# Kernel tuning notes

Hardware: AMD Instinct MI355X
Metric: run time of the kernel (lower is better)

## Reference

```python
import jax, jax.numpy as jnp
import numpy as np

B = 4096   # batch (samples)
V = 64     # num_vars
H = 512    # hidden_dim


def setup_inputs() -> dict:
    key = jax.random.key(0)
    k0, k1, k2, k3 = jax.random.split(key, 4)
    x = jax.random.normal(k0, (B, V), dtype=jnp.float32)
    # learned params: adjacency logits + stacked per-variable 2-layer MLPs
    adj_weights = jax.random.normal(k1, (V, V), dtype=jnp.float32) * 0.1
    W1 = jax.random.normal(k2, (V, V - 1, H), dtype=jnp.float32) * (1.0 / np.sqrt(V - 1))
    b1 = jnp.zeros((V, H), dtype=jnp.float32)
    W2 = jax.random.normal(k3, (V, H), dtype=jnp.float32) * (1.0 / np.sqrt(H))
    b2 = jnp.zeros((V,), dtype=jnp.float32)
    return {"x": x, "adj_weights": adj_weights, "W1": W1, "b1": b1, "W2": W2, "b2": b2}


def reference(x, adj_weights, W1, b1, W2, b2):
    Vn = adj_weights.shape[0]
    # sigmoid adjacency with zeroed diagonal
    adj = jax.nn.sigmoid(adj_weights) * (1.0 - jnp.eye(Vn, dtype=adj_weights.dtype))
    # idx[i, j] = j if j < i else j + 1  -> columns of x excluding variable i
    j = jnp.arange(Vn - 1)
    idx = j[None, :] + (j[None, :] >= jnp.arange(Vn)[:, None])  # [V, V-1] int
    gathered = x[:, idx]                                  # [B, V, V-1]
    w = jnp.take_along_axis(adj, idx, axis=1)             # [V, V-1] (row i, cols != i)
    weighted = gathered * w[None, :, :]                   # [B, V, V-1]
    # batched small MLP per variable
    h = jax.nn.relu(jnp.einsum('bvk,vkh->bvh', weighted, W1) + b1[None])  # [B, V, H]
    out = jnp.einsum('bvh,vh->bv', h, W2) + b2[None]                      # [B, V]
    return out
```

## Files before the change

### kernel.cpp

```cpp
#include <hip/hip_runtime.h>
#include <hip/hip_bf16.h>

constexpr int Bn = 4096;
constexpr int Vn = 64;
constexpr int Hn = 512;

typedef __attribute__((ext_vector_type(8))) short bf16x8;
typedef __attribute__((ext_vector_type(4))) float f32x4;
typedef __attribute__((ext_vector_type(8))) unsigned short u16x8;

union bfcast { u16x8 u; bf16x8 b; };

__device__ __forceinline__ unsigned short f2bf(float f) {
    union { float f; unsigned int u; } x; x.f = f;
    unsigned int u = x.u;
    u += 0x7fffu + ((u >> 16) & 1u);
    return (unsigned short)(u >> 16);
}

__global__ void prep_w1(const float* __restrict__ adjw,
                        const float* __restrict__ W1,
                        unsigned short* __restrict__ bfrag) {
    int nb   = (blockIdx.x & 7) * 128 + (blockIdx.x >> 3);
    int tid  = nb * 256 + threadIdx.x;
    int lane = tid & 63;
    int ks   = (tid >> 6) & 1;
    int nt   = (tid >> 7) & 31;
    int v    = tid >> 12;

    int n     = nt * 16 + (lane & 15);
    int kbase = ks * 32 + ((lane >> 4) << 3);

    u16x8 o;
#pragma unroll
    for (int e = 0; e < 8; ++e) {
        int k = kbase + e;
        float val = 0.f;
        if (k != v) {
            float aw = adjw[v * Vn + k];
            float s  = 1.f / (1.f + __expf(-aw));
            int  j   = k - (k > v);
            val = s * W1[((size_t)(v * (Vn - 1) + j)) * Hn + n];
        }
        o[e] = f2bf(val);
    }
    *reinterpret_cast<u16x8*>(bfrag + (size_t)tid * 8) = o;
}

__global__ __launch_bounds__(256, 4)
void main_k(const float* __restrict__ x,
            const unsigned short* __restrict__ bfrag,
            const float* __restrict__ b1, const float* __restrict__ W2,
            const float* __restrict__ b2, float* __restrict__ out) {
    int wid  = threadIdx.x >> 6;
    int lane = threadIdx.x & 63;
    int nb   = (blockIdx.x & 7) * 128 + (blockIdx.x >> 3);
    int job  = nb * 4 + wid;
    int v    = job >> 6;
    int rg   = job & 63;

    const unsigned short* bpan = bfrag + (size_t)v * 32 * 2 * 512;
    const float* w2row = W2 + v * Hn;
    const float* b1row = b1 + v * Hn;
    int ncol = lane & 15;

    bf16x8 pb0[3], pb1[3];
    float  pw2[3], pbv[3];
#pragma unroll
    for (int p = 0; p < 3; ++p) {
        pb0[p] = *reinterpret_cast<const bf16x8*>(bpan + (size_t)p * 1024 + 0 + lane * 8);
        pb1[p] = *reinterpret_cast<const bf16x8*>(bpan + (size_t)p * 1024 + 512 + lane * 8);
        pw2[p] = w2row[p * 16 + ncol];
        pbv[p] = b1row[p * 16 + ncol];
    }

    bf16x8 a[4][2];
#pragma unroll
    for (int m = 0; m < 4; ++m)
#pragma unroll
        for (int ks = 0; ks < 2; ++ks) {
            int brow  = rg * 64 + m * 16 + (lane & 15);
            int kbase = ks * 32 + ((lane >> 4) << 3);
            const float* xp = x + (size_t)brow * Vn + kbase;
            f32x4 lo = *reinterpret_cast<const f32x4*>(xp);
            f32x4 hi = *reinterpret_cast<const f32x4*>(xp + 4);
            bfcast t;
#pragma unroll
            for (int e = 0; e < 4; ++e) {
                t.u[e]     = f2bf(lo[e]);
                t.u[e + 4] = f2bf(hi[e]);
            }
            a[m][ks] = t.b;
        }

    float partial[4][4] = {};

#pragma unroll
    for (int j = 0; j < 32; ++j) {
        const int cur = j % 3;
        if (j < 29) {
            const int nxt = j % 3;
        }
#pragma unroll
        for (int m = 0; m < 4; ++m) {
            f32x4 c = {pbv[cur], pbv[cur], pbv[cur], pbv[cur]};
            __builtin_amdgcn_s_setprio(1);
            c = __builtin_amdgcn_mfma_f32_16x16x32_bf16(a[m][0], pb0[cur], c, 0, 0, 0);
            c = __builtin_amdgcn_mfma_f32_16x16x32_bf16(a[m][1], pb1[cur], c, 0, 0, 0);
            __builtin_amdgcn_s_setprio(0);
#pragma unroll
            for (int r = 0; r < 4; ++r)
                partial[m][r] = fmaf(fmaxf(c[r], 0.f), pw2[cur], partial[m][r]);
        }
        if (j < 29) {
            pb0[cur] = *reinterpret_cast<const bf16x8*>(
                bpan + (size_t)(j + 3) * 1024 + 0 + lane * 8);
            pb1[cur] = *reinterpret_cast<const bf16x8*>(
                bpan + (size_t)(j + 3) * 1024 + 512 + lane * 8);
            pw2[cur] = w2row[(j + 3) * 16 + ncol];
            pbv[cur] = b1row[(j + 3) * 16 + ncol];
        }
    }

#pragma unroll
    for (int m = 0; m < 4; ++m)
#pragma unroll
        for (int r = 0; r < 4; ++r) {
            float s = partial[m][r];
            s += __shfl_xor(s, 1);
            s += __shfl_xor(s, 2);
            s += __shfl_xor(s, 4);
            s += __shfl_xor(s, 8);
            partial[m][r] = s;
        }

    float b2v = b2[v];
    if ((lane & 15) == 0) {
        int hi = lane >> 4;
#pragma unroll
        for (int m = 0; m < 4; ++m)
#pragma unroll
            for (int r = 0; r < 4; ++r) {
                int row = rg * 64 + m * 16 + hi * 4 + r;
                out[(size_t)row * Vn + v] = partial[m][r] + b2v;
            }
    }
}

extern "C" void kernel_launch(void* const* d_in, const int* in_sizes, int n_in,
                              void* d_out, int out_size, void* d_ws, size_t ws_size,
                              hipStream_t stream) {
    const float* x    = (const float*)d_in[0];
    const float* adjw = (const float*)d_in[1];
    const float* W1   = (const float*)d_in[2];
    const float* b1   = (const float*)d_in[3];
    const float* W2   = (const float*)d_in[4];
    const float* b2   = (const float*)d_in[5];
    float* out = (float*)d_out;

    unsigned short* bfrag = (unsigned short*)d_ws;

    prep_w1<<<1024, 256, 0, stream>>>(adjw, W1, bfrag);
    main_k<<<1024, 256, 0, stream>>>(x, bfrag, b1, W2, b2, out);
}
```

Measured before the change: 35.23 us.

## Stage per-variable W1 panel in LDS shared by eight waves per block

Blocks grow to 512 threads, and each block handles one variable with 8 waves covering 8 row groups. The variable's full 64KB bf16 W1 fragment panel, plus its W2 and b1 rows, is loaded cooperatively into LDS once. The MFMA loop then double-buffers B fragments from LDS instead of triple-buffering per-wave global loads. This cuts redundant global/L2 traffic for the weight panel, at the cost of 68KB of LDS per block, which limits occupancy, and a barrier before compute. The s_setprio hints are also removed.

```diff
diff --git a/kernel.cpp b/kernel.cpp
--- a/kernel.cpp
+++ b/kernel.cpp
@@ -47,32 +47,35 @@
     *reinterpret_cast<u16x8*>(bfrag + (size_t)tid * 8) = o;
 }
 
-__global__ __launch_bounds__(256, 4)
+__global__ __launch_bounds__(512, 4)
 void main_k(const float* __restrict__ x,
             const unsigned short* __restrict__ bfrag,
             const float* __restrict__ b1, const float* __restrict__ W2,
             const float* __restrict__ b2, float* __restrict__ out) {
-    int wid  = threadIdx.x >> 6;
-    int lane = threadIdx.x & 63;
-    int nb   = (blockIdx.x & 7) * 128 + (blockIdx.x >> 3);
-    int job  = nb * 4 + wid;
-    int v    = job >> 6;
-    int rg   = job & 63;
+    __shared__ __align__(16) unsigned char smem[69632];
 
-    const unsigned short* bpan = bfrag + (size_t)v * 32 * 2 * 512;
-    const float* w2row = W2 + v * Hn;
-    const float* b1row = b1 + v * Hn;
-    int ncol = lane & 15;
+    int t    = threadIdx.x;
+    int wid  = t >> 6;
+    int lane = t & 63;
+    int nb   = ((blockIdx.x & 7) << 6) + (blockIdx.x >> 3);
+    int v    = nb >> 3;
+    int rg   = ((nb & 7) << 3) + wid;
 
-    bf16x8 pb0[3], pb1[3];
-    float  pw2[3], pbv[3];
+    const u16x8* gpan = reinterpret_cast<const u16x8*>(bfrag) + (size_t)v * 4096;
+    u16x8 stg[8];
 #pragma unroll
-    for (int p = 0; p < 3; ++p) {
-        pb0[p] = *reinterpret_cast<const bf16x8*>(bpan + (size_t)p * 1024 + 0 + lane * 8);
-        pb1[p] = *reinterpret_cast<const bf16x8*>(bpan + (size_t)p * 1024 + 512 + lane * 8);
-        pw2[p] = w2row[p * 16 + ncol];
-        pbv[p] = b1row[p * 16 + ncol];
-    }
+    for (int i = 0; i < 8; ++i) stg[i] = gpan[i * 512 + t];
+
+    int sel = t >> 7;
+    f32x4 vstg;
+    if (sel == 0)      vstg = reinterpret_cast<const f32x4*>(W2 + v * Hn)[t & 127];
+    else if (sel == 1) vstg = reinterpret_cast<const f32x4*>(b1 + v * Hn)[t & 127];
+
+    u16x8* lpan = reinterpret_cast<u16x8*>(smem);
+#pragma unroll
+    for (int i = 0; i < 8; ++i) lpan[i * 512 + t] = stg[i];
+    if (sel == 0)      reinterpret_cast<f32x4*>(smem + 65536)[t & 127] = vstg;
+    else if (sel == 1) reinterpret_cast<f32x4*>(smem + 67584)[t & 127] = vstg;
 
     bf16x8 a[4][2];
 #pragma unroll
@@ -84,41 +87,48 @@
             const float* xp = x + (size_t)brow * Vn + kbase;
             f32x4 lo = *reinterpret_cast<const f32x4*>(xp);
             f32x4 hi = *reinterpret_cast<const f32x4*>(xp + 4);
-            bfcast t;
+            bfcast tc;
 #pragma unroll
             for (int e = 0; e < 4; ++e) {
-                t.u[e]     = f2bf(lo[e]);
-                t.u[e + 4] = f2bf(hi[e]);
+                tc.u[e]     = f2bf(lo[e]);
+                tc.u[e + 4] = f2bf(hi[e]);
             }
-            a[m][ks] = t.b;
+            a[m][ks] = tc.b;
         }
+
+    __syncthreads();
+
+    const bf16x8* lb  = reinterpret_cast<const bf16x8*>(smem);
+    const float*  w2l = reinterpret_cast<const float*>(smem + 65536);
+    const float*  b1l = reinterpret_cast<const float*>(smem + 67584);
+    int ncol = lane & 15;
+
+    bf16x8 pb0[2], pb1[2];
+    float  pw2[2], pbv[2];
+    pb0[0] = lb[lane];
+    pb1[0] = lb[64 + lane];
+    pw2[0] = w2l[ncol];
+    pbv[0] = b1l[ncol];
 
     float partial[4][4] = {};
 
 #pragma unroll
     for (int j = 0; j < 32; ++j) {
-        const int cur = j % 3;
-        if (j < 29) {
-            const int nxt = j % 3;
+        const int cur = j & 1, nxt = cur ^ 1;
+        if (j < 31) {
+            pb0[nxt] = lb[(j + 1) * 128 + lane];
+            pb1[nxt] = lb[(j + 1) * 128 + 64 + lane];
+            pw2[nxt] = w2l[(j + 1) * 16 + ncol];
+            pbv[nxt] = b1l[(j + 1) * 16 + ncol];
         }
 #pragma unroll
         for (int m = 0; m < 4; ++m) {
             f32x4 c = {pbv[cur], pbv[cur], pbv[cur], pbv[cur]};
-            __builtin_amdgcn_s_setprio(1);
             c = __builtin_amdgcn_mfma_f32_16x16x32_bf16(a[m][0], pb0[cur], c, 0, 0, 0);
             c = __builtin_amdgcn_mfma_f32_16x16x32_bf16(a[m][1], pb1[cur], c, 0, 0, 0);
-            __builtin_amdgcn_s_setprio(0);
 #pragma unroll
             for (int r = 0; r < 4; ++r)
                 partial[m][r] = fmaf(fmaxf(c[r], 0.f), pw2[cur], partial[m][r]);
-        }
-        if (j < 29) {
-            pb0[cur] = *reinterpret_cast<const bf16x8*>(
-                bpan + (size_t)(j + 3) * 1024 + 0 + lane * 8);
-            pb1[cur] = *reinterpret_cast<const bf16x8*>(
-                bpan + (size_t)(j + 3) * 1024 + 512 + lane * 8);
-            pw2[cur] = w2row[(j + 3) * 16 + ncol];
-            pbv[cur] = b1row[(j + 3) * 16 + ncol];
         }
     }
 
@@ -161,5 +171,5 @@
     unsigned short* bfrag = (unsigned short*)d_ws;
 
     prep_w1<<<1024, 256, 0, stream>>>(adjw, W1, bfrag);
-    main_k<<<1024, 256, 0, stream>>>(x, bfrag, b1, W2, b2, out);
+    main_k<<<512, 512, 0, stream>>>(x, bfrag, b1, W2, b2, out);
 }
```

After: 33.51 us. -4.9%, faster.
